# Kernel tuning notes

Measured on AMD Instinct MI355X. Metric: run time of the kernel, lower is better.

Reference implementation:

```python
import jax, jax.numpy as jnp
import numpy as np

B, T, HID = 2, 2048, 1024
H, DK, DV = 8, 128, 128      # num_heads, head_f_dim (key), head_i_dim (value)
LR = 128                     # gate low-rank dim
EPS = 1e-5


def setup_inputs() -> dict:
    key = jax.random.key(0)
    ks = jax.random.split(key, 8)
    def w(k, shape, fan_in):
        return jax.random.normal(k, shape, jnp.float32) / np.float32(np.sqrt(fan_in))
    return {
        "hidden_states": jax.random.normal(ks[0], (B, T, HID), jnp.float32),
        "Wq": w(ks[1], (HID, HID), HID),   # key_dim x hidden
        "Wk": w(ks[2], (HID, HID), HID),
        "Wv": w(ks[3], (HID, HID), HID),   # value_dim x hidden
        "Wg1": w(ks[4], (LR, HID), HID),   # low-rank gate down
        "Wg2": w(ks[5], (HID, LR), LR),    # low-rank gate up
        "g_norm_weight": jnp.ones((HID,), jnp.float32),
        "Wo": w(ks[6], (HID, HID), HID),
    }


def _lightnet_fwd(x, Wq, Wk, Wv, Wg1, Wg2, g_norm_weight, Wo):
    b, t, _ = x.shape
    q = jax.nn.silu(x @ Wq.T).reshape(b, t, H, DK)
    k = (x @ Wk.T).reshape(b, t, H, DK)
    v = (x @ Wv.T).reshape(b, t, H, DV)

    # LightNet gating: normalized keys via logcumsumexp over time
    z = jax.lax.cumlogsumexp(k, axis=1)                 # [b,t,h,dk]
    k = jnp.exp(k - z)                                  # exp-normalized keys
    g = jnp.concatenate([z[:, :1], z[:, :-1]], axis=1) - z  # <= 0; g[:,0]=0

    scale = DK ** -0.5

    # gated linear attention recurrence: S_t = exp(g_t) * S_{t-1} + k_t v_t^T
    def step(S, inp):
        qt, kt, vt, gt = inp                            # [b,h,dk],[b,h,dk],[b,h,dv],[b,h,dk]
        S = jnp.exp(gt)[..., None] * S + kt[..., None] * vt[..., None, :]
        o = jnp.einsum('bhk,bhkv->bhv', qt, S) * scale
        return S, o

    S0 = jnp.zeros((b, H, DK, DV), x.dtype)
    tfirst = lambda a: jnp.moveaxis(a, 1, 0)
    _, oT = jax.lax.scan(step, S0, (tfirst(q), tfirst(k), tfirst(v), tfirst(g)))
    o = jnp.moveaxis(oT, 0, 1).reshape(b, t, H * DV)    # [b,t,hidden]

    # RMSNorm(o) * swish(gate) then output projection
    gate = (x @ Wg1.T) @ Wg2.T
    o = o * jax.lax.rsqrt(jnp.mean(o * o, axis=-1, keepdims=True) + EPS) * g_norm_weight
    o = o * gate * jax.nn.sigmoid(gate)
    return o @ Wo.T


def reference(hidden_states, Wq, Wk, Wv, Wg1, Wg2, g_norm_weight, Wo):
    return _lightnet_fwd(hidden_states, Wq, Wk, Wv, Wg1, Wg2, g_norm_weight, Wo)
```

## Files before the change

kernel.cpp:

```cpp
#include <hip/hip_runtime.h>
#include <hip/hip_bf16.h>
#include <stdint.h>


typedef short short8 __attribute__((ext_vector_type(8)));
typedef float f32x4 __attribute__((ext_vector_type(4)));

#define T_SEQ 2048
#define HIDN  1024
#define SCALE 0.08838834764831845f
#define LDSP  136

__device__ __forceinline__ float blo(unsigned int u){
  union{unsigned int i; float f;} v; v.i = u << 16; return v.f;
}
__device__ __forceinline__ float bhi(unsigned int u){
  union{unsigned int i; float f;} v; v.i = u & 0xffff0000u; return v.f;
}
__device__ __forceinline__ float bu2f(unsigned short u){
  union{unsigned int i; float f;} v; v.i = ((unsigned int)u) << 16; return v.f;
}
__device__ __forceinline__ unsigned short f2bu(float f){
  union{float f; unsigned int i;} v; v.f = f;
  unsigned int x = v.i;
  x += 0x7fffu + ((x >> 16) & 1u);
  return (unsigned short)(x >> 16);
}
__device__ __forceinline__ void async16(const void* g, void* l){
  __builtin_amdgcn_global_load_lds(
      (const __attribute__((address_space(1))) unsigned int*)g,
      (__attribute__((address_space(3))) unsigned int*)l, 16, 0, 0);
}

__global__ __launch_bounds__(256) void convert_all(
    const float* __restrict__ X,  const float* __restrict__ Wq,
    const float* __restrict__ Wk, const float* __restrict__ Wv,
    const float* __restrict__ Wg1,const float* __restrict__ Wg2,
    const float* __restrict__ gnw,const float* __restrict__ Wo,
    unsigned short* __restrict__ base, float* __restrict__ SumSq)
{
  int q = blockIdx.x * 256 + threadIdx.x;
  const float* src; unsigned short* dst; int rel = q;
  if (rel < 1048576)            { src = X;   dst = base;            }
  else if ((rel -= 1048576) < 262144) { src = Wq;  dst = base + 4194304; }
  else if ((rel -=  262144) < 262144) { src = Wk;  dst = base + 5242880; }
  else if ((rel -=  262144) < 262144) { src = Wv;  dst = base + 6291456; }
  else if ((rel -=  262144) < 262144) { src = Wo;  dst = base + 7340032; }
  else if ((rel -=  262144) <  32768) { src = Wg1; dst = base + 8388608; }
  else if ((rel -=   32768) <  32768) { src = Wg2; dst = base + 8519680; }
  else if ((rel -=   32768) <    256) { src = gnw; dst = base + 8650752; }
  else { rel -= 256;
    ((float4*)SumSq)[rel] = make_float4(0.f,0.f,0.f,0.f); return; }
  float4 v = ((const float4*)src)[rel];
  ushort4 o; o.x=f2bu(v.x); o.y=f2bu(v.y); o.z=f2bu(v.z); o.w=f2bu(v.w);
  ((ushort4*)dst)[rel] = o;
}

__device__ __forceinline__ void gemm_core(
    const unsigned short* __restrict__ A, const unsigned short* __restrict__ B,
    int K, int row0, int col0,
    unsigned short* sA, unsigned short* sB, f32x4 acc[4][4], int tid)
{
  const int lane = tid & 63;
  const int wm = (tid >> 6) & 1, wn = tid >> 7;
  const int wb = tid & 192;
  for (int k0 = 0; k0 < K; k0 += 64){
    __syncthreads();
#pragma unroll
    for (int r = 0; r < 4; ++r){
      int idx  = r*256 + tid;
      int mrow = idx >> 3;
      int kc   = ((idx & 7) ^ (mrow & 7)) * 8;
      async16(A + (size_t)(row0 + mrow)*K + k0 + kc,
              sA + (size_t)(r*256 + wb)*8);
      async16(B + (size_t)(col0 + mrow)*K + k0 + kc,
              sB + (size_t)(r*256 + wb)*8);
    }
    __syncthreads();
#pragma unroll
    for (int h = 0; h < 2; ++h){
      short8 av[4], bv[4];
#pragma unroll
      for (int i=0;i<4;i++){
        int ra = wm*64 + i*16 + (lane&15);
        av[i] = *(const short8*)(sA + (size_t)ra*64
                                 + (((h*4 + (lane>>4)) ^ (ra & 7)) * 8));
      }
#pragma unroll
      for (int j=0;j<4;j++){
        int rb = wn*64 + j*16 + (lane&15);
        bv[j] = *(const short8*)(sB + (size_t)rb*64
                                 + (((h*4 + (lane>>4)) ^ (rb & 7)) * 8));
      }
#pragma unroll
      for (int i=0;i<4;i++)
#pragma unroll
        for (int j=0;j<4;j++)
          acc[i][j] = __builtin_amdgcn_mfma_f32_16x16x32_bf16(av[i], bv[j], acc[i][j], 0, 0, 0);
    }
  }
}

__device__ __forceinline__ void epilogue_lds(
    f32x4 acc[4][4], int row0, int col0, int tid, int ldc, int act,
    unsigned short* __restrict__ Cb, unsigned short* sC)
{
  const int lane = tid & 63;
  const int wm = (tid >> 6) & 1, wn = tid >> 7;
#pragma unroll
  for (int p=0;p<4;p++){
    __syncthreads();
    if (wm == (p>>1)){
#pragma unroll
      for (int ii=0; ii<2; ii++){
        int i = (p&1)*2 + ii;
        int lr = i*16 + ((lane>>4)<<2) - (p&1)*32;
#pragma unroll
        for (int j=0;j<4;j++){
          int col = wn*64 + j*16 + (lane&15);
#pragma unroll
          for (int r=0;r<4;r++){
            float v = acc[i][j][r];
            if (act == 1) v = v / (1.f + __expf(-v));
            else if (act == 2) v = __expf(v);
            sC[(lr+r)*128 + col] = f2bu(v);
          }
        }
      }
    }
    __syncthreads();
#pragma unroll
    for (int c = tid; c < 512; c += 256){
      int rr = c >> 4, off = (c & 15)*8;
      *(uint4*)&Cb[(size_t)(row0 + p*32 + rr)*ldc + col0 + off] =
          *(const uint4*)&sC[rr*128 + off];
    }
  }
}

__device__ __forceinline__ void epilogue_f32(
    f32x4 acc[4][4], int row0, int col0, int tid, int ldc,
    float* __restrict__ Cf)
{
  const int lane = tid & 63;
  const int wm = (tid >> 6) & 1, wn = tid >> 7;
#pragma unroll
  for (int i=0;i<4;i++){
    int rbase = row0 + wm*64 + i*16 + ((lane>>4)<<2);
#pragma unroll
    for (int j=0;j<4;j++){
      int col = col0 + wn*64 + j*16 + (lane&15);
#pragma unroll
      for (int r=0;r<4;r++)
        Cf[(size_t)(rbase + r)*ldc + col] = acc[i][j][r];
    }
  }
}

__global__ __launch_bounds__(256, 4) void proj_kernel(
    const unsigned short* __restrict__ X,
    const unsigned short* __restrict__ Wq, const unsigned short* __restrict__ Wk,
    const unsigned short* __restrict__ Wv, const unsigned short* __restrict__ Wg1,
    unsigned short* __restrict__ Qb, unsigned short* __restrict__ Eb,
    unsigned short* __restrict__ Vb, unsigned short* __restrict__ G1b)
{
  __shared__ unsigned short sA[128*64], sB[128*64];
  int tid = threadIdx.x;
  int which = blockIdx.y >> 3;
  const unsigned short* Bp = (which==0)?Wq:(which==1)?Wk:(which==2)?Wv:Wg1;
  int row0 = blockIdx.x * 128;
  int col0 = (which==3) ? 0 : (blockIdx.y & 7) * 128;
  f32x4 acc[4][4] = {};
  gemm_core(X, Bp, HIDN, row0, col0, sA, sB, acc, tid);
  if      (which==0) epilogue_lds(acc,row0,col0,tid,HIDN,1,Qb, sA);
  else if (which==1) epilogue_lds(acc,row0,col0,tid,HIDN,2,Eb, sA);
  else if (which==2) epilogue_lds(acc,row0,col0,tid,HIDN,0,Vb, sA);
  else               epilogue_lds(acc,row0,col0,tid,128 ,0,G1b,sA);
}

__global__ __launch_bounds__(256, 4) void gemm_bt(
    const unsigned short* __restrict__ A, const unsigned short* __restrict__ B,
    int K, int ldc, int act, float* __restrict__ Cf,
    unsigned short* __restrict__ Cb)
{
  __shared__ unsigned short sA[128*64], sB[128*64];
  int tid = threadIdx.x;
  int row0 = blockIdx.x * 128, col0 = blockIdx.y * 128;
  f32x4 acc[4][4] = {};
  gemm_core(A, B, K, row0, col0, sA, sB, acc, tid);
  if (Cb) epilogue_lds(acc, row0, col0, tid, ldc, act, Cb, sA);
  else    epilogue_f32(acc, row0, col0, tid, ldc, Cf);
}

__global__ __launch_bounds__(512, 2) void attn_pass1(
    const unsigned short* __restrict__ Eb, const unsigned short* __restrict__ Vb,
    unsigned short* __restrict__ U, float* __restrict__ Esum)
{
  __shared__ unsigned short Vt[128*LDSP], Et[128*LDSP];
  __shared__ float seg_part[4*128];
  int tid = threadIdx.x;
  const int lane = tid & 63, quad = lane >> 4;
  const int w = tid >> 6, wm = w & 3, wn = w >> 2;
  const int Rb = wm*32, Cb = wn*64;
  int bh = blockIdx.x >> 4, ch = blockIdx.x & 15;
  int b = bh >> 3, h = bh & 7;
  size_t rowbase = (size_t)(b*T_SEQ + ch*128)*HIDN + h*128;

#pragma unroll
  for (int i=0;i<4;i++){
    int u = tid + i*512; int t = u >> 4, kc = (u & 15)*8;
    int trot = (t + kc) & 127;
    unsigned short tmp[8];
    *(uint4*)tmp = *(const uint4*)&Vb[rowbase + (size_t)t*HIDN + kc];
#pragma unroll
    for (int j=0;j<8;j++) Vt[(kc+j)*LDSP + trot] = tmp[j];
    *(uint4*)tmp = *(const uint4*)&Eb[rowbase + (size_t)t*HIDN + kc];
#pragma unroll
    for (int j=0;j<8;j++) Et[(kc+j)*LDSP + trot] = tmp[j];
  }
  __syncthreads();

  {
    int seg = tid >> 7, k = tid & 127;
    float s = 0.f;
    for (int c = seg*32; c < seg*32+32; ++c)
      s += bu2f(Et[k*LDSP + ((c + (k & 120)) & 127)]);
    seg_part[seg*128 + k] = s;
  }
  __syncthreads();
  if (tid < 128)
    Esum[(size_t)blockIdx.x*128 + tid] =
        seg_part[tid] + seg_part[128+tid] + seg_part[256+tid] + seg_part[384+tid];

  f32x4 acc[2][4] = {};
  short8 av[2], bv[4];
#pragma unroll
  for (int s0=0; s0<128; s0+=32){
#pragma unroll
    for (int i=0;i<2;i++){
      int ra = Rb + i*16 + (lane&15);
      av[i] = *(const short8*)(Vt + ra*LDSP + ((s0 + quad*8 + (ra & 120)) & 127));
    }
#pragma unroll
    for (int j=0;j<4;j++){
      int rb = Cb + j*16 + (lane&15);
      bv[j] = *(const short8*)(Et + rb*LDSP + ((s0 + quad*8 + (rb & 120)) & 127));
    }
#pragma unroll
    for (int i=0;i<2;i++)
#pragma unroll
      for (int j=0;j<4;j++)
        acc[i][j] = __builtin_amdgcn_mfma_f32_16x16x32_bf16(av[i], bv[j], acc[i][j], 0,0,0);
  }
  __syncthreads();

#pragma unroll
  for (int i=0;i<2;i++)
#pragma unroll
    for (int j=0;j<4;j++){
      int k = Cb + j*16 + (lane&15);
#pragma unroll
      for (int r=0;r<4;r++){
        int v = Rb + i*16 + quad*4 + r;
        Et[v*LDSP + k] = f2bu(acc[i][j][r]);
      }
    }
  __syncthreads();
  unsigned short* Ub = U + (size_t)blockIdx.x*16384;
#pragma unroll
  for (int i=0;i<4;i++){
    int u = tid + i*512; int v = u >> 4, kc = (u & 15)*8;
    *(uint4*)&Ub[v*128 + kc] = *(const uint4*)&Et[v*LDSP + kc];
  }
}

__global__ __launch_bounds__(256) void attn_pass2(
    unsigned short* __restrict__ U, float* __restrict__ Esum)
{
  int bh = blockIdx.x >> 4, sl = blockIdx.x & 15;
  int p = sl*1024 + threadIdx.x*4;
  float r0=0.f, r1=0.f, r2=0.f, r3=0.f;
  for (int c=0;c<16;c++){
    ushort4* ptr = (ushort4*)&U[(size_t)(bh*16 + c)*16384 + p];
    ushort4 t = *ptr;
    ushort4 w;
    w.x=f2bu(r0); w.y=f2bu(r1); w.z=f2bu(r2); w.w=f2bu(r3);
    *ptr = w;
    r0 += bu2f(t.x); r1 += bu2f(t.y); r2 += bu2f(t.z); r3 += bu2f(t.w);
  }
  if (sl == 0 && threadIdx.x < 128){
    float r = 0.f;
    for (int c=0;c<16;c++){
      float* q = &Esum[(size_t)(bh*16 + c)*128 + threadIdx.x];
      float t = *q; *q = r; r += t;
    }
  }
}

__global__ __launch_bounds__(512, 4) void attn_pass3(
    const unsigned short* __restrict__ Eb, const unsigned short* __restrict__ Qb,
    const unsigned short* __restrict__ Vb, const unsigned short* __restrict__ U,
    const float* __restrict__ Esum, unsigned short* __restrict__ Oatt,
    float* __restrict__ SumSq)
{
  __shared__ unsigned short smem[2*128*LDSP];
  __shared__ float seg_part[4*128];
  unsigned short* bufA = smem;
  unsigned short* bufB = smem + 128*LDSP;

  int tid = threadIdx.x;
  const int lane = tid & 63, quad = lane >> 4;
  const int w = tid >> 6, wm = w & 3, wn = w >> 2;
  const int Rb = wm*32, Cb = wn*64;
  int bh = blockIdx.x >> 4, ch = blockIdx.x & 15;
  int b = bh >> 3, h = bh & 7;
  size_t rowbase = (size_t)(b*T_SEQ + ch*128)*HIDN + h*128;
  const unsigned short* Ublk = U + (size_t)blockIdx.x*16384;

#pragma unroll
  for (int i=0;i<4;i++){
    int u = tid + i*512; int t = u >> 4, kc = (u & 15)*8;
    *(uint4*)&bufA[t*LDSP + kc] = *(const uint4*)&Qb[rowbase + (size_t)t*HIDN + kc];
    *(uint4*)&bufB[t*LDSP + kc] = *(const uint4*)&Eb[rowbase + (size_t)t*HIDN + kc];
  }
  __syncthreads();

  {
    int col = tid & 127, seg = tid >> 7;
    float psum = 0.f;
    for (int s = seg*32; s < seg*32+32; ++s) psum += bu2f(bufB[s*LDSP + col]);
    seg_part[seg*128 + col] = psum;
    __syncthreads();
    float run = Esum[(size_t)blockIdx.x*128 + col];
    for (int ss=0; ss<4; ++ss) if (ss < seg) run += seg_part[ss*128 + col];
    for (int s = seg*32; s < seg*32+32; ++s){
      run += bu2f(bufB[s*LDSP + col]);
      float q = bu2f(bufA[s*LDSP + col]);
      bufA[s*LDSP + col] = f2bu(q * SCALE * __builtin_amdgcn_rcpf(run));
    }
  }
  __syncthreads();

  f32x4 accO[2][4] = {}, accP[2][4] = {};
  short8 av[2], bv[4];
#pragma unroll
  for (int k0=0; k0<128; k0+=32){
#pragma unroll
    for (int i=0;i<2;i++)
      av[i] = *(const short8*)(bufA + (Rb + i*16 + (lane&15))*LDSP + k0 + quad*8);
#pragma unroll
    for (int j=0;j<4;j++)
      bv[j] = *(const short8*)(Ublk + (size_t)(Cb + j*16 + (lane&15))*128 + k0 + quad*8);
#pragma unroll
    for (int i=0;i<2;i++)
#pragma unroll
      for (int j=0;j<4;j++)
        accO[i][j] = __builtin_amdgcn_mfma_f32_16x16x32_bf16(av[i], bv[j], accO[i][j], 0,0,0);
#pragma unroll
    for (int j=0;j<4;j++)
      bv[j] = *(const short8*)(bufB + (Cb + j*16 + (lane&15))*LDSP + k0 + quad*8);
#pragma unroll
    for (int i=0;i<2;i++)
#pragma unroll
      for (int j=0;j<4;j++)
        accP[i][j] = __builtin_amdgcn_mfma_f32_16x16x32_bf16(av[i], bv[j], accP[i][j], 0,0,0);
  }
  __syncthreads();

#pragma unroll
  for (int i=0;i<2;i++){
#pragma unroll
    for (int j=0;j<4;j++){
      int s = Cb + j*16 + (lane&15);
#pragma unroll
      for (int r=0;r<4;r++){
        int t = Rb + i*16 + quad*4 + r;
        bufA[t*LDSP + s] = f2bu(s <= t ? accP[i][j][r] : 0.f);
      }
    }
  }
#pragma unroll
  for (int i=0;i<4;i++){
    int u = tid + i*512; int t = u >> 4, kc = (u & 15)*8;
    int trot = (t + kc) & 127;
    unsigned short tmp[8];
    *(uint4*)tmp = *(const uint4*)&Vb[rowbase + (size_t)t*HIDN + kc];
#pragma unroll
    for (int j=0;j<8;j++) bufB[(kc+j)*LDSP + trot] = tmp[j];
  }
  __syncthreads();

#pragma unroll
  for (int k0=0; k0<128; k0+=32){
#pragma unroll
    for (int i=0;i<2;i++)
      av[i] = *(const short8*)(bufA + (Rb + i*16 + (lane&15))*LDSP + k0 + quad*8);
#pragma unroll
    for (int j=0;j<4;j++){
      int rb = Cb + j*16 + (lane&15);
      bv[j] = *(const short8*)(bufB + rb*LDSP + ((k0 + quad*8 + (rb & 120)) & 127));
    }
#pragma unroll
    for (int i=0;i<2;i++)
#pragma unroll
      for (int j=0;j<4;j++)
        accO[i][j] = __builtin_amdgcn_mfma_f32_16x16x32_bf16(av[i], bv[j], accO[i][j], 0,0,0);
  }
  __syncthreads();

#pragma unroll
  for (int i=0;i<2;i++){
#pragma unroll
    for (int j=0;j<4;j++){
      int v = Cb + j*16 + (lane&15);
#pragma unroll
      for (int r=0;r<4;r++){
        int t = Rb + i*16 + quad*4 + r;
        bufA[t*LDSP + v] = f2bu(accO[i][j][r]);
      }
    }
  }
  __syncthreads();

  {
    int seg = tid >> 7, row = tid & 127;
    float s = 0.f;
    for (int c = seg*32; c < seg*32+32; ++c){
      float x = bu2f(bufA[row*LDSP + c]); s += x*x;
    }
    seg_part[seg*128 + row] = s;
  }
#pragma unroll
  for (int i=0;i<4;i++){
    int u = tid + i*512; int t = u >> 4, kc = (u & 15)*8;
    *(uint4*)&Oatt[rowbase + (size_t)t*HIDN + kc] = *(const uint4*)&bufA[t*LDSP + kc];
  }
  __syncthreads();
  if (tid < 128){
    float s = seg_part[tid] + seg_part[128+tid] + seg_part[256+tid] + seg_part[384+tid];
    atomicAdd(&SumSq[(size_t)b*T_SEQ + ch*128 + tid], s);
  }
}

__global__ __launch_bounds__(256) void norm_gate2(
    const unsigned short* __restrict__ Oatt, const unsigned short* __restrict__ Gt,
    const unsigned short* __restrict__ gnw, const float* __restrict__ SumSq,
    unsigned short* __restrict__ Onorm)
{
  int row = blockIdx.x, tid = threadIdx.x;
  float rstd = rsqrtf(SumSq[row] * (1.f/1024.f) + 1e-5f);
  ushort4 o4 = *(const ushort4*)&Oatt[(size_t)row*HIDN + tid*4];
  ushort4 g4 = *(const ushort4*)&Gt  [(size_t)row*HIDN + tid*4];
  ushort4 w4 = *(const ushort4*)&gnw[tid*4];
  ushort4 r4;
  r4.x = f2bu(bu2f(o4.x) * rstd * bu2f(w4.x) * bu2f(g4.x));
  r4.y = f2bu(bu2f(o4.y) * rstd * bu2f(w4.y) * bu2f(g4.y));
  r4.z = f2bu(bu2f(o4.z) * rstd * bu2f(w4.z) * bu2f(g4.z));
  r4.w = f2bu(bu2f(o4.w) * rstd * bu2f(w4.w) * bu2f(g4.w));
  *(ushort4*)&Onorm[(size_t)row*HIDN + tid*4] = r4;
}

extern "C" void kernel_launch(void* const* d_in, const int* in_sizes, int n_in,
                              void* d_out, int out_size, void* d_ws, size_t ws_size,
                              hipStream_t stream) {
  unsigned short* wsS = (unsigned short*)d_ws;

  unsigned short* Xc   = wsS;
  unsigned short* Wqc  = wsS + 4194304;
  unsigned short* Wkc  = wsS + 5242880;
  unsigned short* Wvc  = wsS + 6291456;
  unsigned short* Woc  = wsS + 7340032;
  unsigned short* Wg1c = wsS + 8388608;
  unsigned short* Wg2c = wsS + 8519680;
  unsigned short* gnwc = wsS + 8650752;
  unsigned short* Qb   = wsS + 8651776;
  unsigned short* Eb   = wsS + 12846080;
  unsigned short* Vb   = wsS + 17040384;
  unsigned short* G1b  = wsS + 21234688;
  unsigned short* Gt   = wsS + 21758976;
  unsigned short* Ub   = wsS + 25953280;
  unsigned short* Oattb= wsS + 30147584;
  float*          Esum = (float*)(wsS + 34341888);
  float*          SumSq= (float*)(wsS + 34407424);
  unsigned short* Onorm = Qb;

  convert_all<<<8453, 256, 0, stream>>>(
      (const float*)d_in[0], (const float*)d_in[1], (const float*)d_in[2],
      (const float*)d_in[3], (const float*)d_in[4], (const float*)d_in[5],
      (const float*)d_in[6], (const float*)d_in[7], wsS, SumSq);

  proj_kernel<<<dim3(32,25), 256, 0, stream>>>(Xc, Wqc, Wkc, Wvc, Wg1c, Qb, Eb, Vb, G1b);
  gemm_bt   <<<dim3(32,8),  256, 0, stream>>>(G1b, Wg2c, 128, HIDN, 1, nullptr, Gt);
  attn_pass1<<<256, 512, 0, stream>>>(Eb, Vb, Ub, Esum);
  attn_pass2<<<256, 256, 0, stream>>>(Ub, Esum);
  attn_pass3<<<256, 512, 0, stream>>>(Eb, Qb, Vb, Ub, Esum, Oattb, SumSq);
  norm_gate2<<<4096, 256, 0, stream>>>(Oattb, Gt, gnwc, SumSq, Onorm);
  gemm_bt   <<<dim3(32,8),  256, 0, stream>>>(Onorm, Woc, HIDN, HIDN, 0,
                                              (float*)d_out, nullptr);
}
```

Before: 196.1 us.

## Split attention chunks over value halves and fold prefix-state scan into pass3

```diff
diff --git a/kernel.cpp b/kernel.cpp
--- a/kernel.cpp
+++ b/kernel.cpp
@@ -192,17 +192,19 @@
   else    epilogue_f32(acc, row0, col0, tid, ldc, Cf);
 }
 
-__global__ __launch_bounds__(512, 2) void attn_pass1(
+__global__ __launch_bounds__(512, 4) void attn_pass1(
     const unsigned short* __restrict__ Eb, const unsigned short* __restrict__ Vb,
     unsigned short* __restrict__ U, float* __restrict__ Esum)
 {
-  __shared__ unsigned short Vt[128*LDSP], Et[128*LDSP];
+  __shared__ unsigned short Et[128*LDSP];
+  __shared__ unsigned short Vt[64*LDSP];
   __shared__ float seg_part[4*128];
   int tid = threadIdx.x;
-  const int lane = tid & 63, quad = lane >> 4;
+  const int lane = tid & 63, quad = lane >> 4, l15 = lane & 15;
   const int w = tid >> 6, wm = w & 3, wn = w >> 2;
-  const int Rb = wm*32, Cb = wn*64;
-  int bh = blockIdx.x >> 4, ch = blockIdx.x & 15;
+  const int Rb = wm*16, Cb = wn*64;
+  int bx = blockIdx.x;
+  int bh = bx >> 5, ch = (bx >> 1) & 15, vh = bx & 1;
   int b = bh >> 3, h = bh & 7;
   size_t rowbase = (size_t)(b*T_SEQ + ch*128)*HIDN + h*128;
 
@@ -211,16 +213,22 @@
     int u = tid + i*512; int t = u >> 4, kc = (u & 15)*8;
     int trot = (t + kc) & 127;
     unsigned short tmp[8];
-    *(uint4*)tmp = *(const uint4*)&Vb[rowbase + (size_t)t*HIDN + kc];
-#pragma unroll
-    for (int j=0;j<8;j++) Vt[(kc+j)*LDSP + trot] = tmp[j];
     *(uint4*)tmp = *(const uint4*)&Eb[rowbase + (size_t)t*HIDN + kc];
 #pragma unroll
     for (int j=0;j<8;j++) Et[(kc+j)*LDSP + trot] = tmp[j];
   }
-  __syncthreads();
-
-  {
+#pragma unroll
+  for (int i=0;i<2;i++){
+    int u = tid + i*512; int t = u >> 3, kc8 = (u & 7)*8;
+    int trot = (t + kc8) & 127;
+    unsigned short tmp[8];
+    *(uint4*)tmp = *(const uint4*)&Vb[rowbase + (size_t)t*HIDN + vh*64 + kc8];
+#pragma unroll
+    for (int j=0;j<8;j++) Vt[(kc8+j)*LDSP + trot] = tmp[j];
+  }
+  __syncthreads();
+
+  if (vh == 0){
     int seg = tid >> 7, k = tid & 127;
     float s = 0.f;
     for (int c = seg*32; c < seg*32+32; ++c)
@@ -228,72 +236,44 @@
     seg_part[seg*128 + k] = s;
   }
   __syncthreads();
-  if (tid < 128)
-    Esum[(size_t)blockIdx.x*128 + tid] =
+  if (vh == 0 && tid < 128)
+    Esum[(size_t)(bx>>1)*128 + tid] =
         seg_part[tid] + seg_part[128+tid] + seg_part[256+tid] + seg_part[384+tid];
 
-  f32x4 acc[2][4] = {};
-  short8 av[2], bv[4];
+  f32x4 acc[4] = {};
 #pragma unroll
   for (int s0=0; s0<128; s0+=32){
-#pragma unroll
-    for (int i=0;i<2;i++){
-      int ra = Rb + i*16 + (lane&15);
-      av[i] = *(const short8*)(Vt + ra*LDSP + ((s0 + quad*8 + (ra & 120)) & 127));
+    short8 av, bv[4];
+    {
+      int ra = Rb + l15;
+      av = *(const short8*)(Vt + ra*LDSP + ((s0 + quad*8 + (ra & 120)) & 127));
     }
 #pragma unroll
     for (int j=0;j<4;j++){
-      int rb = Cb + j*16 + (lane&15);
+      int rb = Cb + j*16 + l15;
       bv[j] = *(const short8*)(Et + rb*LDSP + ((s0 + quad*8 + (rb & 120)) & 127));
     }
 #pragma unroll
-    for (int i=0;i<2;i++)
-#pragma unroll
-      for (int j=0;j<4;j++)
-        acc[i][j] = __builtin_amdgcn_mfma_f32_16x16x32_bf16(av[i], bv[j], acc[i][j], 0,0,0);
-  }
-  __syncthreads();
-
-#pragma unroll
-  for (int i=0;i<2;i++)
-#pragma unroll
-    for (int j=0;j<4;j++){
-      int k = Cb + j*16 + (lane&15);
-#pragma unroll
-      for (int r=0;r<4;r++){
-        int v = Rb + i*16 + quad*4 + r;
-        Et[v*LDSP + k] = f2bu(acc[i][j][r]);
-      }
-    }
-  __syncthreads();
-  unsigned short* Ub = U + (size_t)blockIdx.x*16384;
-#pragma unroll
-  for (int i=0;i<4;i++){
+    for (int j=0;j<4;j++)
+      acc[j] = __builtin_amdgcn_mfma_f32_16x16x32_bf16(av, bv[j], acc[j], 0,0,0);
+  }
+  __syncthreads();
+
+#pragma unroll
+  for (int j=0;j<4;j++){
+    int k = Cb + j*16 + l15;
+#pragma unroll
+    for (int r=0;r<4;r++){
+      int v = Rb + quad*4 + r;
+      Et[v*LDSP + k] = f2bu(acc[j][r]);
+    }
+  }
+  __syncthreads();
+  unsigned short* Ub = U + ((size_t)(bx>>1) << 14);
+#pragma unroll
+  for (int i=0;i<2;i++){
     int u = tid + i*512; int v = u >> 4, kc = (u & 15)*8;
-    *(uint4*)&Ub[v*128 + kc] = *(const uint4*)&Et[v*LDSP + kc];
-  }
-}
-
-__global__ __launch_bounds__(256) void attn_pass2(
-    unsigned short* __restrict__ U, float* __restrict__ Esum)
-{
-  int bh = blockIdx.x >> 4, sl = blockIdx.x & 15;
-  int p = sl*1024 + threadIdx.x*4;
-  float r0=0.f, r1=0.f, r2=0.f, r3=0.f;
-  for (int c=0;c<16;c++){
-    ushort4* ptr = (ushort4*)&U[(size_t)(bh*16 + c)*16384 + p];
-    ushort4 t = *ptr;
-    ushort4 w;
-    w.x=f2bu(r0); w.y=f2bu(r1); w.z=f2bu(r2); w.w=f2bu(r3);
-    *ptr = w;
-    r0 += bu2f(t.x); r1 += bu2f(t.y); r2 += bu2f(t.z); r3 += bu2f(t.w);
-  }
-  if (sl == 0 && threadIdx.x < 128){
-    float r = 0.f;
-    for (int c=0;c<16;c++){
-      float* q = &Esum[(size_t)(bh*16 + c)*128 + threadIdx.x];
-      float t = *q; *q = r; r += t;
-    }
+    *(uint4*)&Ub[(size_t)(vh*64 + v)*128 + kc] = *(const uint4*)&Et[v*LDSP + kc];
   }
 }
 
@@ -303,19 +283,20 @@
     const float* __restrict__ Esum, unsigned short* __restrict__ Oatt,
     float* __restrict__ SumSq)
 {
-  __shared__ unsigned short smem[2*128*LDSP];
+  __shared__ unsigned short bufA[128*LDSP];
+  __shared__ unsigned short bufB[128*LDSP];
   __shared__ float seg_part[4*128];
-  unsigned short* bufA = smem;
-  unsigned short* bufB = smem + 128*LDSP;
 
   int tid = threadIdx.x;
-  const int lane = tid & 63, quad = lane >> 4;
+  const int lane = tid & 63, quad = lane >> 4, l15 = lane & 15;
   const int w = tid >> 6, wm = w & 3, wn = w >> 2;
-  const int Rb = wm*32, Cb = wn*64;
-  int bh = blockIdx.x >> 4, ch = blockIdx.x & 15;
+  const int Rb = wm*32;
+  const int CbP = wn*64;
+  const int CbO = wn*32;
+  int bx = blockIdx.x;
+  int bh = bx >> 5, ch = (bx >> 1) & 15, vh = bx & 1;
   int b = bh >> 3, h = bh & 7;
   size_t rowbase = (size_t)(b*T_SEQ + ch*128)*HIDN + h*128;
-  const unsigned short* Ublk = U + (size_t)blockIdx.x*16384;
 
 #pragma unroll
   for (int i=0;i<4;i++){
@@ -331,7 +312,8 @@
     for (int s = seg*32; s < seg*32+32; ++s) psum += bu2f(bufB[s*LDSP + col]);
     seg_part[seg*128 + col] = psum;
     __syncthreads();
-    float run = Esum[(size_t)blockIdx.x*128 + col];
+    float run = 0.f;
+    for (int c = 0; c < ch; ++c) run += Esum[(size_t)(bh*16 + c)*128 + col];
     for (int ss=0; ss<4; ++ss) if (ss < seg) run += seg_part[ss*128 + col];
     for (int s = seg*32; s < seg*32+32; ++s){
       run += bu2f(bufB[s*LDSP + col]);
@@ -341,29 +323,33 @@
   }
   __syncthreads();
 
-  f32x4 accO[2][4] = {}, accP[2][4] = {};
-  short8 av[2], bv[4];
-#pragma unroll
-  for (int k0=0; k0<128; k0+=32){
+  f32x4 accP[2][4] = {}, accO[2][2] = {};
+#pragma unroll
+  for (int k0i=0; k0i<4; ++k0i){
+    const int k0 = k0i*32;
+    short8 av[2], bv[4];
 #pragma unroll
     for (int i=0;i<2;i++)
-      av[i] = *(const short8*)(bufA + (Rb + i*16 + (lane&15))*LDSP + k0 + quad*8);
+      av[i] = *(const short8*)(bufA + (Rb + i*16 + l15)*LDSP + k0 + quad*8);
 #pragma unroll
     for (int j=0;j<4;j++)
-      bv[j] = *(const short8*)(Ublk + (size_t)(Cb + j*16 + (lane&15))*128 + k0 + quad*8);
-#pragma unroll
-    for (int i=0;i<2;i++)
-#pragma unroll
-      for (int j=0;j<4;j++)
-        accO[i][j] = __builtin_amdgcn_mfma_f32_16x16x32_bf16(av[i], bv[j], accO[i][j], 0,0,0);
-#pragma unroll
-    for (int j=0;j<4;j++)
-      bv[j] = *(const short8*)(bufB + (Cb + j*16 + (lane&15))*LDSP + k0 + quad*8);
+      bv[j] = *(const short8*)(bufB + (CbP + j*16 + l15)*LDSP + k0 + quad*8);
 #pragma unroll
     for (int i=0;i<2;i++)
 #pragma unroll
       for (int j=0;j<4;j++)
         accP[i][j] = __builtin_amdgcn_mfma_f32_16x16x32_bf16(av[i], bv[j], accP[i][j], 0,0,0);
+    for (int c=0; c<ch; ++c){
+      const unsigned short* Uc = U + (((size_t)(bh*16 + c)) << 14)
+                               + (size_t)(vh*64 + CbO)*128;
+      short8 u0 = *(const short8*)(Uc + (size_t)l15*128 + k0 + quad*8);
+      short8 u1 = *(const short8*)(Uc + (size_t)(16 + l15)*128 + k0 + quad*8);
+#pragma unroll
+      for (int i=0;i<2;i++){
+        accO[i][0] = __builtin_amdgcn_mfma_f32_16x16x32_bf16(av[i], u0, accO[i][0], 0,0,0);
+        accO[i][1] = __builtin_amdgcn_mfma_f32_16x16x32_bf16(av[i], u1, accO[i][1], 0,0,0);
+      }
+    }
   }
   __syncthreads();
 
@@ -371,7 +357,7 @@
   for (int i=0;i<2;i++){
 #pragma unroll
     for (int j=0;j<4;j++){
-      int s = Cb + j*16 + (lane&15);
+      int s = CbP + j*16 + l15;
 #pragma unroll
       for (int r=0;r<4;r++){
         int t = Rb + i*16 + quad*4 + r;
@@ -380,30 +366,31 @@
     }
   }
 #pragma unroll
-  for (int i=0;i<4;i++){
-    int u = tid + i*512; int t = u >> 4, kc = (u & 15)*8;
-    int trot = (t + kc) & 127;
+  for (int i=0;i<2;i++){
+    int u = tid + i*512; int t = u >> 3, kc8 = (u & 7)*8;
+    int trot = (t + kc8) & 127;
     unsigned short tmp[8];
-    *(uint4*)tmp = *(const uint4*)&Vb[rowbase + (size_t)t*HIDN + kc];
-#pragma unroll
-    for (int j=0;j<8;j++) bufB[(kc+j)*LDSP + trot] = tmp[j];
+    *(uint4*)tmp = *(const uint4*)&Vb[rowbase + (size_t)t*HIDN + vh*64 + kc8];
+#pragma unroll
+    for (int j=0;j<8;j++) bufB[(kc8+j)*LDSP + trot] = tmp[j];
   }
   __syncthreads();
 
 #pragma unroll
   for (int k0=0; k0<128; k0+=32){
+    short8 av[2], bv[2];
 #pragma unroll
     for (int i=0;i<2;i++)
-      av[i] = *(const short8*)(bufA + (Rb + i*16 + (lane&15))*LDSP + k0 + quad*8);
-#pragma unroll
-    for (int j=0;j<4;j++){
-      int rb = Cb + j*16 + (lane&15);
-      bv[j] = *(const short8*)(bufB + rb*LDSP + ((k0 + quad*8 + (rb & 120)) & 127));
+      av[i] = *(const short8*)(bufA + (Rb + i*16 + l15)*LDSP + k0 + quad*8);
+#pragma unroll
+    for (int j=0;j<2;j++){
+      int rv = CbO + j*16 + l15;
+      bv[j] = *(const short8*)(bufB + rv*LDSP + ((k0 + quad*8 + (rv & 120)) & 127));
     }
 #pragma unroll
     for (int i=0;i<2;i++)
 #pragma unroll
-      for (int j=0;j<4;j++)
+      for (int j=0;j<2;j++)
         accO[i][j] = __builtin_amdgcn_mfma_f32_16x16x32_bf16(av[i], bv[j], accO[i][j], 0,0,0);
   }
   __syncthreads();
@@ -411,12 +398,12 @@
 #pragma unroll
   for (int i=0;i<2;i++){
 #pragma unroll
-    for (int j=0;j<4;j++){
-      int v = Cb + j*16 + (lane&15);
+    for (int j=0;j<2;j++){
+      int vv = CbO + j*16 + l15;
 #pragma unroll
       for (int r=0;r<4;r++){
         int t = Rb + i*16 + quad*4 + r;
-        bufA[t*LDSP + v] = f2bu(accO[i][j][r]);
+        bufA[t*LDSP + vv] = f2bu(accO[i][j][r]);
       }
     }
   }
@@ -425,15 +412,16 @@
   {
     int seg = tid >> 7, row = tid & 127;
     float s = 0.f;
-    for (int c = seg*32; c < seg*32+32; ++c){
+    for (int c = seg*16; c < seg*16+16; ++c){
       float x = bu2f(bufA[row*LDSP + c]); s += x*x;
     }
     seg_part[seg*128 + row] = s;
   }
 #pragma unroll
-  for (int i=0;i<4;i++){
-    int u = tid + i*512; int t = u >> 4, kc = (u & 15)*8;
-    *(uint4*)&Oatt[rowbase + (size_t)t*HIDN + kc] = *(const uint4*)&bufA[t*LDSP + kc];
+  for (int i=0;i<2;i++){
+    int u = tid + i*512; int t = u >> 3, kc8 = (u & 7)*8;
+    *(uint4*)&Oatt[rowbase + (size_t)t*HIDN + vh*64 + kc8] =
+        *(const uint4*)&bufA[t*LDSP + kc8];
   }
   __syncthreads();
   if (tid < 128){
@@ -491,9 +479,8 @@
 
   proj_kernel<<<dim3(32,25), 256, 0, stream>>>(Xc, Wqc, Wkc, Wvc, Wg1c, Qb, Eb, Vb, G1b);
   gemm_bt   <<<dim3(32,8),  256, 0, stream>>>(G1b, Wg2c, 128, HIDN, 1, nullptr, Gt);
-  attn_pass1<<<256, 512, 0, stream>>>(Eb, Vb, Ub, Esum);
-  attn_pass2<<<256, 256, 0, stream>>>(Ub, Esum);
-  attn_pass3<<<256, 512, 0, stream>>>(Eb, Qb, Vb, Ub, Esum, Oattb, SumSq);
+  attn_pass1<<<512, 512, 0, stream>>>(Eb, Vb, Ub, Esum);
+  attn_pass3<<<512, 512, 0, stream>>>(Eb, Qb, Vb, Ub, Esum, Oattb, SumSq);
   norm_gate2<<<4096, 256, 0, stream>>>(Oattb, Gt, gnwc, SumSq, Onorm);
   gemm_bt   <<<dim3(32,8),  256, 0, stream>>>(Onorm, Woc, HIDN, HIDN, 0,
                                               (float*)d_out, nullptr);
```

Result: slower. 237.8 us (+21.3%).
